# Optimization experiments

Measured on AMD Instinct MI355X. Metric: run time of the kernel, lower is better.

Reference implementation:

```python
import jax, jax.numpy as jnp
import numpy as np

B, I, C, U, S = 256, 128, 1024, 32, 16  # batch, in_units, in_channels, num_units, unit_size
NUM_ITERS = 3

def setup_inputs() -> dict:
    key = jax.random.key(0)
    k1, k2 = jax.random.split(key)
    x = jax.random.normal(k1, (B, I, C), dtype=jnp.float32)
    W = jax.random.normal(k2, (1, C, U, S, I), dtype=jnp.float32)
    return {"x": x, "W": W}

def _squash(s):
    # s: (b, u, s); original squashes over dim=2 of (b,1,U,S,1), i.e. the num_units axis
    mag_sq = jnp.sum(s * s, axis=1, keepdims=True)
    mag = jnp.sqrt(mag_sq)
    return mag_sq / (1.0 + mag_sq) * (s / mag)

def reference(x, W):
    # x: (b, in_units, in_channels) -> (b, c, i)
    xT = jnp.swapaxes(x, 1, 2)
    # u_hat[b,c,u,s] = sum_i W[0,c,u,s,i] * xT[b,c,i]  (replaces torch.cat broadcast + matmul)
    u_hat = jnp.einsum('cusi,bci->bcus', W[0], xT)
    b_ij = jnp.zeros((1, C, U, 1), dtype=x.dtype)
    v_j = None
    for _ in range(NUM_ITERS):
        # softmax over axis 0 of size 1 -> all ones (faithful to original quirk)
        c_ij = jax.nn.softmax(b_ij, axis=0)
        s_j = jnp.einsum('cu,bcus->bus', c_ij[0, :, :, 0], u_hat)
        v_j = _squash(s_j)
        # agreement: mean over batch of <u_hat, v_j> along unit_size
        u_vj = jnp.einsum('bcus,bus->cu', u_hat, v_j) / B
        b_ij = b_ij + u_vj[None, :, :, None]
    return v_j[..., None]  # (b, num_units, unit_size, 1) == v_j.squeeze(1)
```

## Files before the change

### kernel.cpp

```cpp
#include <hip/hip_runtime.h>
#include <hip/hip_bf16.h>
#include <stdint.h>

#define B_DIM 256
#define I_DIM 128
#define C_DIM 1024
#define N_DIM 512
#define KC    (C_DIM * I_DIM)
#define WC    (N_DIM * I_DIM)

typedef __bf16 bf16;
typedef __attribute__((ext_vector_type(4))) __bf16 bf16x4;
typedef __attribute__((ext_vector_type(8))) __bf16 bf16x8;
typedef __attribute__((ext_vector_type(4))) float f32x4;

__device__ __forceinline__ void async_copy16(const void* g, void* l) {
  __builtin_amdgcn_global_load_lds(
      (const __attribute__((address_space(1))) uint32_t*)g,
      (__attribute__((address_space(3))) uint32_t*)l, 16, 0, 0);
}

__global__ void __launch_bounds__(256)
transpose_cast(const float* __restrict__ x, bf16* __restrict__ xT) {
  __shared__ float tile[64][65];
  const int c0 = blockIdx.x * 64;
  const int i0 = blockIdx.y * 64;
  const int b  = blockIdx.z;
  const int t  = threadIdx.x;
  const int sub = t >> 4;
  const int cg  = t & 15;
  const float* xb = x + (size_t)b * (I_DIM * C_DIM);
#pragma unroll
  for (int r = 0; r < 4; ++r) {
    const int i = r * 16 + sub;
    const float4 v = *(const float4*)&xb[(size_t)(i0 + i) * C_DIM + c0 + cg * 4];
    tile[i][cg * 4 + 0] = v.x; tile[i][cg * 4 + 1] = v.y;
    tile[i][cg * 4 + 2] = v.z; tile[i][cg * 4 + 3] = v.w;
  }
  __syncthreads();
  bf16* xTb = xT + (size_t)b * KC;
#pragma unroll
  for (int r = 0; r < 2; ++r) {
    const int c  = r * 32 + (t >> 3);
    const int ic = (t & 7) * 8;
    bf16x8 o;
#pragma unroll
    for (int k = 0; k < 8; ++k) o[k] = (bf16)tile[ic + k][c];
    *(bf16x8*)&xTb[(size_t)(c0 + c) * I_DIM + i0 + ic] = o;
  }
}

__device__ __forceinline__ void stage_step(
    const bf16* __restrict__ xT, const float* __restrict__ W,
    short* Asl, float* Wsl, int tid, int c, int h, int n0) {
  const int ch = tid & 7;
  const size_t abase = (size_t)c * I_DIM + h * 64;
#pragma unroll
  for (int p = 0; p < 4; ++p) {
    const int m   = p * 64 + (tid >> 3);
    const int csw = ch ^ (m & 7);
    async_copy16(xT + (size_t)m * KC + abase + csw * 8,
                 &Asl[(p * 512 + tid) * 8]);
  }
  const int s = tid & 15;
  const size_t wbase = (size_t)c * WC + h * 64;
#pragma unroll
  for (int p = 0; p < 2; ++p) {
    const int n   = p * 32 + (tid >> 4);
    const int ssw = s ^ (n & 7);
    async_copy16(W + wbase + (size_t)(n0 + n) * I_DIM + ssw * 4,
                 &Wsl[(p * 512 + tid) * 4]);
  }
}

__device__ __forceinline__ void compute_step(
    const short* Asl, const float* Wsl,
    int wm, int wn, int l15, int lq, f32x4 (&acc)[4][2]) {
#pragma unroll
  for (int ks = 0; ks < 2; ++ks) {
    bf16x8 a[4];
#pragma unroll
    for (int mt = 0; mt < 4; ++mt) {
      const int m  = wm * 64 + mt * 16 + l15;
      const int ch = (ks * 4 + lq) ^ (l15 & 7);
      a[mt] = *(const bf16x8*)&Asl[m * 64 + ch * 8];
    }
    bf16x8 b[2];
#pragma unroll
    for (int nt = 0; nt < 2; ++nt) {
      const int n  = wn * 32 + nt * 16 + l15;
      const int s0 = (ks * 8 + lq * 2)     ^ (l15 & 7);
      const int s1 = (ks * 8 + lq * 2 + 1) ^ (l15 & 7);
      const f32x4 lo = *(const f32x4*)&Wsl[n * 64 + s0 * 4];
      const f32x4 hi = *(const f32x4*)&Wsl[n * 64 + s1 * 4];
      bf16x8 bb;
      bb[0] = (bf16)lo[0]; bb[1] = (bf16)lo[1];
      bb[2] = (bf16)lo[2]; bb[3] = (bf16)lo[3];
      bb[4] = (bf16)hi[0]; bb[5] = (bf16)hi[1];
      bb[6] = (bf16)hi[2]; bb[7] = (bf16)hi[3];
      b[nt] = bb;
    }
#pragma unroll
    for (int mt = 0; mt < 4; ++mt)
#pragma unroll
      for (int nt = 0; nt < 2; ++nt)
        acc[mt][nt] = __builtin_amdgcn_mfma_f32_16x16x32_bf16(
            a[mt], b[nt], acc[mt][nt], 0, 0, 0);
  }
}

__global__ void __launch_bounds__(512, 2)
gemm_kernel(const bf16* __restrict__ xT, const float* __restrict__ W,
            float* __restrict__ sj) {
  __shared__ short As[3][B_DIM * 64];
  __shared__ float Ws[3][64 * 64];
  const int tid  = threadIdx.x;
  const int lane = tid & 63;
  const int wave = tid >> 6;
  const int wm   = wave >> 1;
  const int wn   = wave & 1;
  const int l15  = lane & 15;
  const int lq   = lane >> 4;

  const int g   = blockIdx.x;
  const int n0  = ((g >> 3) & 7) * 64;
  const int cch = (g & 7) * 4 + (g >> 6);
  const int c0  = cch * 32;

  f32x4 acc[4][2] = {};

  short *Aa = As[0], *Ab = As[1], *Ac = As[2];
  float *Wa = Ws[0], *Wb = Ws[1], *Wc = Ws[2];

  stage_step(xT, W, Aa, Wa, tid, c0, 0, n0);
  stage_step(xT, W, Ab, Wb, tid, c0, 1, n0);

#pragma unroll 1
  for (int t = 0; t < 62; ++t) {
    const int tn = t + 2;
    stage_step(xT, W, Ac, Wc, tid, c0 + (tn >> 1), tn & 1, n0);
    asm volatile("s_waitcnt vmcnt(12)" ::: "memory");
    __builtin_amdgcn_sched_barrier(0);
    __builtin_amdgcn_s_barrier();
    compute_step(Aa, Wa, wm, wn, l15, lq, acc);
    __builtin_amdgcn_s_barrier();
    short* ta = Aa; Aa = Ab; Ab = Ac; Ac = ta;
    float* tw = Wa; Wa = Wb; Wb = Wc; Wc = tw;
  }
  asm volatile("s_waitcnt vmcnt(6)" ::: "memory");
  __builtin_amdgcn_sched_barrier(0);
  __builtin_amdgcn_s_barrier();
  compute_step(Aa, Wa, wm, wn, l15, lq, acc);
  asm volatile("s_waitcnt vmcnt(0)" ::: "memory");
  __builtin_amdgcn_sched_barrier(0);
  __builtin_amdgcn_s_barrier();
  compute_step(Ab, Wb, wm, wn, l15, lq, acc);

#pragma unroll
  for (int mt = 0; mt < 4; ++mt) {
#pragma unroll
    for (int nt = 0; nt < 2; ++nt) {
      const int n = n0 + wn * 32 + nt * 16 + l15;
#pragma unroll
      for (int r = 0; r < 4; ++r) {
        const int brow = wm * 64 + mt * 16 + lq * 4 + r;
        atomicAdd(&sj[(size_t)brow * N_DIM + n], acc[mt][nt][r]);
      }
    }
  }
}

__global__ void __launch_bounds__(512)
squash_kernel(const float* __restrict__ sj, float* __restrict__ out) {
  __shared__ float sm[512];
  const int b = blockIdx.x;
  const int t = threadIdx.x;
  const float v = sj[(size_t)b * N_DIM + t];
  sm[t] = v * v;
  __syncthreads();
#pragma unroll
  for (int off = 256; off >= 16; off >>= 1) {
    if (t < off) sm[t] += sm[t + off];
    __syncthreads();
  }
  const float msq   = sm[t & 15];
  const float scale = sqrtf(msq) / (1.0f + msq);
  out[(size_t)b * N_DIM + t] = v * scale;
}

extern "C" void kernel_launch(void* const* d_in, const int* in_sizes, int n_in,
                              void* d_out, int out_size, void* d_ws, size_t ws_size,
                              hipStream_t stream) {
  const float* x = (const float*)d_in[0];
  const float* W = (const float*)d_in[1];
  float* out = (float*)d_out;

  bf16*  xT = (bf16*)d_ws;
  float* sj = (float*)((char*)d_ws + (size_t)B_DIM * KC * sizeof(bf16));

  hipMemsetAsync(sj, 0, (size_t)B_DIM * N_DIM * sizeof(float), stream);
  transpose_cast<<<dim3(C_DIM / 64, I_DIM / 64, B_DIM), 256, 0, stream>>>(x, xT);
  gemm_kernel<<<dim3(256), 512, 0, stream>>>(xT, W, sj);
  squash_kernel<<<B_DIM, 512, 0, stream>>>(sj, out);
}
```

Measured before the change: 492.7 us.

## Widen GEMM N-tile to 128, use channel-major x layout and double buffering

Measured after the change: 477.9 us. 3.0% less time.

```diff
diff --git a/kernel.cpp b/kernel.cpp
--- a/kernel.cpp
+++ b/kernel.cpp
@@ -8,9 +8,9 @@
 #define N_DIM 512
 #define KC    (C_DIM * I_DIM)
 #define WC    (N_DIM * I_DIM)
+#define BI    (B_DIM * I_DIM)
 
 typedef __bf16 bf16;
-typedef __attribute__((ext_vector_type(4))) __bf16 bf16x4;
 typedef __attribute__((ext_vector_type(8))) __bf16 bf16x8;
 typedef __attribute__((ext_vector_type(4))) float f32x4;
 
@@ -21,7 +21,7 @@
 }
 
 __global__ void __launch_bounds__(256)
-transpose_cast(const float* __restrict__ x, bf16* __restrict__ xT) {
+transpose_cast(const float* __restrict__ x, bf16* __restrict__ xc) {
   __shared__ float tile[64][65];
   const int c0 = blockIdx.x * 64;
   const int i0 = blockIdx.y * 64;
@@ -38,7 +38,6 @@
     tile[i][cg * 4 + 2] = v.z; tile[i][cg * 4 + 3] = v.w;
   }
   __syncthreads();
-  bf16* xTb = xT + (size_t)b * KC;
 #pragma unroll
   for (int r = 0; r < 2; ++r) {
     const int c  = r * 32 + (t >> 3);
@@ -46,53 +45,51 @@
     bf16x8 o;
 #pragma unroll
     for (int k = 0; k < 8; ++k) o[k] = (bf16)tile[ic + k][c];
-    *(bf16x8*)&xTb[(size_t)(c0 + c) * I_DIM + i0 + ic] = o;
+    *(bf16x8*)&xc[(size_t)(c0 + c) * BI + (size_t)b * I_DIM + i0 + ic] = o;
   }
 }
 
 __device__ __forceinline__ void stage_step(
-    const bf16* __restrict__ xT, const float* __restrict__ W,
+    const bf16* __restrict__ xc, const float* __restrict__ W,
     short* Asl, float* Wsl, int tid, int c, int h, int n0) {
-  const int ch = tid & 7;
-  const size_t abase = (size_t)c * I_DIM + h * 64;
+  const size_t abase = (size_t)c * BI + h * 64;
 #pragma unroll
   for (int p = 0; p < 4; ++p) {
-    const int m   = p * 64 + (tid >> 3);
-    const int csw = ch ^ (m & 7);
-    async_copy16(xT + (size_t)m * KC + abase + csw * 8,
-                 &Asl[(p * 512 + tid) * 8]);
+    const int g  = p * 512 + tid;
+    const int b  = g >> 3;
+    const int cs = (g & 7) ^ (b & 7);
+    async_copy16(xc + abase + (size_t)b * I_DIM + cs * 8, Asl + (size_t)g * 8);
   }
-  const int s = tid & 15;
-  const size_t wbase = (size_t)c * WC + h * 64;
+  const size_t wbase = (size_t)c * WC + (size_t)n0 * I_DIM + h * 64;
 #pragma unroll
-  for (int p = 0; p < 2; ++p) {
-    const int n   = p * 32 + (tid >> 4);
-    const int ssw = s ^ (n & 7);
-    async_copy16(W + wbase + (size_t)(n0 + n) * I_DIM + ssw * 4,
-                 &Wsl[(p * 512 + tid) * 4]);
+  for (int p = 0; p < 4; ++p) {
+    const int g  = p * 512 + tid;
+    const int n  = g >> 4;
+    const int qs = (g & 15) ^ (n & 15);
+    async_copy16(W + wbase + (size_t)n * I_DIM + qs * 4, Wsl + (size_t)g * 4);
   }
 }
 
 __device__ __forceinline__ void compute_step(
-    const short* Asl, const float* Wsl,
-    int wm, int wn, int l15, int lq, f32x4 (&acc)[4][2]) {
+    const short* As, const float* Wl,
+    int wm, int wn2, int l15, int lq, f32x4 (&acc)[8][2]) {
+  const int m7 = l15 & 7;
 #pragma unroll
-  for (int ks = 0; ks < 2; ++ks) {
-    bf16x8 a[4];
+  for (int ksl = 0; ksl < 2; ++ksl) {
+    bf16x8 a[8];
 #pragma unroll
-    for (int mt = 0; mt < 4; ++mt) {
-      const int m  = wm * 64 + mt * 16 + l15;
-      const int ch = (ks * 4 + lq) ^ (l15 & 7);
-      a[mt] = *(const bf16x8*)&Asl[m * 64 + ch * 8];
+    for (int mt = 0; mt < 8; ++mt) {
+      const int m  = wm * 128 + mt * 16 + l15;
+      const int st = (ksl * 4 + lq) ^ m7;
+      a[mt] = *(const bf16x8*)&As[m * 64 + st * 8];
     }
     bf16x8 b[2];
 #pragma unroll
     for (int nt = 0; nt < 2; ++nt) {
-      const int n  = wn * 32 + nt * 16 + l15;
-      const int s0 = (ks * 8 + lq * 2)     ^ (l15 & 7);
-      const int s1 = (ks * 8 + lq * 2 + 1) ^ (l15 & 7);
-      const f32x4 lo = *(const f32x4*)&Wsl[n * 64 + s0 * 4];
-      const f32x4 hi = *(const f32x4*)&Wsl[n * 64 + s1 * 4];
+      const int n  = wn2 * 32 + nt * 16 + l15;
+      const int q0 = ksl * 8 + lq * 2;
+      const f32x4 lo = *(const f32x4*)&Wl[n * 64 + ((q0 ^ l15) * 4)];
+      const f32x4 hi = *(const f32x4*)&Wl[n * 64 + (((q0 + 1) ^ l15) * 4)];
       bf16x8 bb;
       bb[0] = (bf16)lo[0]; bb[1] = (bf16)lo[1];
       bb[2] = (bf16)lo[2]; bb[3] = (bf16)lo[3];
@@ -101,7 +98,7 @@
       b[nt] = bb;
     }
 #pragma unroll
-    for (int mt = 0; mt < 4; ++mt)
+    for (int mt = 0; mt < 8; ++mt)
 #pragma unroll
       for (int nt = 0; nt < 2; ++nt)
         acc[mt][nt] = __builtin_amdgcn_mfma_f32_16x16x32_bf16(
@@ -110,60 +107,51 @@
 }
 
 __global__ void __launch_bounds__(512, 2)
-gemm_kernel(const bf16* __restrict__ xT, const float* __restrict__ W,
+gemm_kernel(const bf16* __restrict__ xc, const float* __restrict__ W,
             float* __restrict__ sj) {
-  __shared__ short As[3][B_DIM * 64];
-  __shared__ float Ws[3][64 * 64];
+  __shared__ short As[2][B_DIM * 64];
+  __shared__ float Wl[2][128 * 64];
   const int tid  = threadIdx.x;
   const int lane = tid & 63;
-  const int wave = tid >> 6;
-  const int wm   = wave >> 1;
-  const int wn   = wave & 1;
+  const int wv   = tid >> 6;
+  const int wm   = wv >> 2;
+  const int wn2  = wv & 3;
   const int l15  = lane & 15;
   const int lq   = lane >> 4;
 
-  const int g   = blockIdx.x;
-  const int n0  = ((g >> 3) & 7) * 64;
-  const int cch = (g & 7) * 4 + (g >> 6);
-  const int c0  = cch * 32;
+  const int g     = blockIdx.x;
+  const int chunk = (g & 7) * 8 + ((g >> 3) & 7);
+  const int nb    = g >> 6;
+  const int n0    = nb * 128;
+  const int c0    = chunk * 16;
 
-  f32x4 acc[4][2] = {};
+  f32x4 acc[8][2] = {};
 
-  short *Aa = As[0], *Ab = As[1], *Ac = As[2];
-  float *Wa = Ws[0], *Wb = Ws[1], *Wc = Ws[2];
-
-  stage_step(xT, W, Aa, Wa, tid, c0, 0, n0);
-  stage_step(xT, W, Ab, Wb, tid, c0, 1, n0);
+  stage_step(xc, W, As[0], Wl[0], tid, c0, 0, n0);
 
 #pragma unroll 1
-  for (int t = 0; t < 62; ++t) {
-    const int tn = t + 2;
-    stage_step(xT, W, Ac, Wc, tid, c0 + (tn >> 1), tn & 1, n0);
-    asm volatile("s_waitcnt vmcnt(12)" ::: "memory");
+  for (int t = 0; t < 31; ++t) {
+    const int tn = t + 1;
+    stage_step(xc, W, As[tn & 1], Wl[tn & 1], tid, c0 + (tn >> 1), tn & 1, n0);
+    asm volatile("s_waitcnt vmcnt(8)" ::: "memory");
     __builtin_amdgcn_sched_barrier(0);
     __builtin_amdgcn_s_barrier();
-    compute_step(Aa, Wa, wm, wn, l15, lq, acc);
+    compute_step(As[t & 1], Wl[t & 1], wm, wn2, l15, lq, acc);
     __builtin_amdgcn_s_barrier();
-    short* ta = Aa; Aa = Ab; Ab = Ac; Ac = ta;
-    float* tw = Wa; Wa = Wb; Wb = Wc; Wc = tw;
   }
-  asm volatile("s_waitcnt vmcnt(6)" ::: "memory");
-  __builtin_amdgcn_sched_barrier(0);
-  __builtin_amdgcn_s_barrier();
-  compute_step(Aa, Wa, wm, wn, l15, lq, acc);
   asm volatile("s_waitcnt vmcnt(0)" ::: "memory");
   __builtin_amdgcn_sched_barrier(0);
   __builtin_amdgcn_s_barrier();
-  compute_step(Ab, Wb, wm, wn, l15, lq, acc);
+  compute_step(As[1], Wl[1], wm, wn2, l15, lq, acc);
 
 #pragma unroll
-  for (int mt = 0; mt < 4; ++mt) {
+  for (int mt = 0; mt < 8; ++mt) {
 #pragma unroll
     for (int nt = 0; nt < 2; ++nt) {
-      const int n = n0 + wn * 32 + nt * 16 + l15;
+      const int n = n0 + wn2 * 32 + nt * 16 + l15;
 #pragma unroll
       for (int r = 0; r < 4; ++r) {
-        const int brow = wm * 64 + mt * 16 + lq * 4 + r;
+        const int brow = wm * 128 + mt * 16 + lq * 4 + r;
         atomicAdd(&sj[(size_t)brow * N_DIM + n], acc[mt][nt][r]);
       }
     }
@@ -195,11 +183,11 @@
   const float* W = (const float*)d_in[1];
   float* out = (float*)d_out;
 
-  bf16*  xT = (bf16*)d_ws;
-  float* sj = (float*)((char*)d_ws + (size_t)B_DIM * KC * sizeof(bf16));
+  bf16*  xc = (bf16*)d_ws;
+  float* sj = (float*)((char*)d_ws + (size_t)KC * B_DIM * sizeof(bf16));
 
   hipMemsetAsync(sj, 0, (size_t)B_DIM * N_DIM * sizeof(float), stream);
-  transpose_cast<<<dim3(C_DIM / 64, I_DIM / 64, B_DIM), 256, 0, stream>>>(x, xT);
-  gemm_kernel<<<dim3(256), 512, 0, stream>>>(xT, W, sj);
+  transpose_cast<<<dim3(C_DIM / 64, I_DIM / 64, B_DIM), 256, 0, stream>>>(x, xc);
+  gemm_kernel<<<dim3(256), 512, 0, stream>>>(xc, W, sj);
   squash_kernel<<<B_DIM, 512, 0, stream>>>(sj, out);
 }
```
